# Kernel tuning notes

Hardware: AMD Instinct MI355X
Metric: run time of the kernel (lower is better)

The kernel has to match this reference:

```python
import jax, jax.numpy as jnp
import numpy as np
import math

N_NODES = 100000
N_EDGES = 3200000
NFEAT = 512
NHID = 256
NCLASS = 16
NLAYERS = 8
LAMDA = 0.5
ALPHA = 0.1


def setup_inputs() -> dict:
    key = jax.random.key(0)
    ks = jax.random.split(key, 10)
    x = jax.random.normal(ks[0], (N_NODES, NFEAT), dtype=jnp.float32)
    edge_src = jax.random.randint(ks[1], (N_EDGES,), 0, N_NODES, dtype=jnp.int32)
    edge_dst = jax.random.randint(ks[2], (N_EDGES,), 0, N_NODES, dtype=jnp.int32)
    edge_w = jax.random.uniform(ks[3], (N_EDGES,), dtype=jnp.float32)
    # fcs[0]: Linear(nfeat, nhidden); fcs[1]: Linear(nhidden, nclass)
    s0 = 1.0 / math.sqrt(NFEAT)
    w0 = jax.random.uniform(ks[4], (NFEAT, NHID), minval=-s0, maxval=s0, dtype=jnp.float32)
    b0 = jax.random.uniform(ks[5], (NHID,), minval=-s0, maxval=s0, dtype=jnp.float32)
    # conv weights: uniform(-1/sqrt(out_features), +), out_features = nhidden
    sc = 1.0 / math.sqrt(NHID)
    conv_w = jax.random.uniform(ks[6], (NLAYERS, NHID, NHID), minval=-sc, maxval=sc, dtype=jnp.float32)
    w1 = jax.random.uniform(ks[7], (NHID, NCLASS), minval=-sc, maxval=sc, dtype=jnp.float32)
    b1 = jax.random.uniform(ks[8], (NCLASS,), minval=-sc, maxval=sc, dtype=jnp.float32)
    return {"x": x, "edge_src": edge_src, "edge_dst": edge_dst, "edge_w": edge_w,
            "w0": w0, "b0": b0, "conv_w": conv_w, "w1": w1, "b1": b1}


def _spmm(edge_src, edge_dst, edge_w, h):
    # torch.spmm(adj, h): out[i] = sum_j adj[i,j] * h[j], adj in COO (dst=row, src=col)
    msgs = edge_w[:, None] * h[edge_src]            # [E, H] irregular gather
    return jax.ops.segment_sum(msgs, edge_dst, num_segments=h.shape[0])


def reference(x, edge_src, edge_dst, edge_w, w0, b0, conv_w, w1, b1):
    # eval mode: F.dropout is identity
    h = jax.nn.relu(x @ w0 + b0)                    # [N, NHID]
    h0 = h
    for i in range(NLAYERS):
        theta = math.log(LAMDA / (i + 1) + 1.0)
        hi = _spmm(edge_src, edge_dst, edge_w, h)   # sparse aggregate
        support = (1.0 - ALPHA) * hi + ALPHA * h0   # initial residual (GCNII)
        out = theta * (support @ conv_w[i]) + (1.0 - theta) * support
        h = jax.nn.relu(out + h)                    # layer residual
    return jax.nn.sigmoid(h @ w1 + b1)              # [N, NCLASS]
```

## Files before the change

### kernel.cpp

```cpp
#include <hip/hip_runtime.h>
#include <math.h>

#define N_NODES 100000
#define N_EDGES 3200000
#define NFEAT 512
#define NHID 256
#define NCLASS 16
#define NLAYERS 8

#define SCAN_CHUNK 1024
#define NB ((N_NODES + SCAN_CHUNK - 1) / SCAN_CHUNK)

__global__ void k_hist(const int* __restrict__ dst, int* __restrict__ cnt) {
  int i = blockIdx.x * 256 + threadIdx.x;
  if (i < N_EDGES) atomicAdd(&cnt[dst[i]], 1);
}

__global__ void k_blocksum(const int* __restrict__ cnt, int* __restrict__ bs) {
  __shared__ int red[256];
  int b = blockIdx.x, t = threadIdx.x;
  int s = 0;
  int base = b * SCAN_CHUNK;
  for (int j = 0; j < 4; ++j) {
    int i = base + t + j * 256;
    if (i < N_NODES) s += cnt[i];
  }
  red[t] = s;
  __syncthreads();
  for (int off = 128; off > 0; off >>= 1) {
    if (t < off) red[t] += red[t + off];
    __syncthreads();
  }
  if (t == 0) bs[b] = red[0];
}

__global__ void k_scan_top(int* __restrict__ bs, int* __restrict__ rp) {
  if (threadIdx.x == 0) {
    int run = 0;
    for (int b = 0; b < NB; ++b) { int v = bs[b]; bs[b] = run; run += v; }
    rp[N_NODES] = run;
  }
}

__global__ void k_scan_write(const int* __restrict__ cnt, const int* __restrict__ bs,
                             int* __restrict__ rp) {
  __shared__ int tot[256];
  int b = blockIdx.x, t = threadIdx.x;
  int base = b * SCAN_CHUNK + t * 4;
  int v0 = 0, v1 = 0, v2 = 0, v3 = 0;
  if (base + 0 < N_NODES) v0 = cnt[base + 0];
  if (base + 1 < N_NODES) v1 = cnt[base + 1];
  if (base + 2 < N_NODES) v2 = cnt[base + 2];
  if (base + 3 < N_NODES) v3 = cnt[base + 3];
  int tsum = v0 + v1 + v2 + v3;
  tot[t] = tsum;
  __syncthreads();
  for (int off = 1; off < 256; off <<= 1) {
    int v = 0;
    if (t >= off) v = tot[t - off];
    __syncthreads();
    if (t >= off) tot[t] += v;
    __syncthreads();
  }
  int excl = tot[t] - tsum + bs[b];
  if (base + 0 < N_NODES) rp[base + 0] = excl;
  if (base + 1 < N_NODES) rp[base + 1] = excl + v0;
  if (base + 2 < N_NODES) rp[base + 2] = excl + v0 + v1;
  if (base + 3 < N_NODES) rp[base + 3] = excl + v0 + v1 + v2;
}

__global__ void k_fill(const int* __restrict__ src, const int* __restrict__ dst,
                       const float* __restrict__ w, const int* __restrict__ rp,
                       int* __restrict__ fill, int* __restrict__ col,
                       float* __restrict__ val) {
  int i = blockIdx.x * 256 + threadIdx.x;
  if (i < N_EDGES) {
    int d = dst[i];
    int pos = rp[d] + atomicAdd(&fill[d], 1);
    col[pos] = src[i];
    val[pos] = w[i];
  }
}

__global__ __launch_bounds__(256)
void k_spmm_half(const int* __restrict__ rp, const int* __restrict__ col,
                 const float* __restrict__ val, const float* __restrict__ h,
                 const float* __restrict__ h0, float* __restrict__ sup, int f0) {
  int wave = threadIdx.x >> 6;
  int lane = threadIdx.x & 63;
  int node = blockIdx.x * 4 + wave;
  if (node >= N_NODES) return;
  int e0 = rp[node], e1 = rp[node + 1];
  const float2* __restrict__ hv = (const float2*)h;
  int fo = (f0 >> 1) + lane;

  float2 a0 = make_float2(0.f, 0.f);
  float2 a1 = make_float2(0.f, 0.f);
  float2 a2 = make_float2(0.f, 0.f);
  float2 a3 = make_float2(0.f, 0.f);

  int e = e0;
  for (; e + 4 <= e1; e += 4) {
    int s0 = col[e], s1 = col[e + 1], s2 = col[e + 2], s3 = col[e + 3];
    float w0 = val[e], w1 = val[e + 1], w2 = val[e + 2], w3 = val[e + 3];
    float2 v0 = hv[(size_t)s0 * 128 + fo];
    float2 v1 = hv[(size_t)s1 * 128 + fo];
    float2 v2 = hv[(size_t)s2 * 128 + fo];
    float2 v3 = hv[(size_t)s3 * 128 + fo];
    a0.x += w0 * v0.x; a0.y += w0 * v0.y;
    a1.x += w1 * v1.x; a1.y += w1 * v1.y;
    a2.x += w2 * v2.x; a2.y += w2 * v2.y;
    a3.x += w3 * v3.x; a3.y += w3 * v3.y;
  }
  for (; e < e1; ++e) {
    int s0 = col[e];
    float w0 = val[e];
    float2 v0 = hv[(size_t)s0 * 128 + fo];
    a0.x += w0 * v0.x; a0.y += w0 * v0.y;
  }

  float2 acc;
  acc.x = (a0.x + a1.x) + (a2.x + a3.x);
  acc.y = (a0.y + a1.y) + (a2.y + a3.y);

  float2 z = ((const float2*)h0)[(size_t)node * 128 + fo];
  float2 o;
  o.x = 0.9f * acc.x + 0.1f * z.x;
  o.y = 0.9f * acc.y + 0.1f * z.y;
  ((float2*)sup)[(size_t)node * 128 + fo] = o;
}

template <int MODE>
__global__ __launch_bounds__(256)
void k_gemm(const float* __restrict__ A, const float* __restrict__ W, int K,
            const float* __restrict__ bias, const float* __restrict__ hin,
            float* __restrict__ out1, float* __restrict__ out2, float theta) {
  __shared__ float As[16][128];
  __shared__ float Bs[16][128];
  int bm = blockIdx.x * 128, bn = blockIdx.y * 128;
  int tid = threadIdx.x;
  int tx = tid & 15, ty = tid >> 4;
  float acc[8][8];
#pragma unroll
  for (int i = 0; i < 8; ++i)
#pragma unroll
    for (int j = 0; j < 8; ++j) acc[i][j] = 0.f;

  for (int kc = 0; kc < K; kc += 16) {
#pragma unroll
    for (int it = 0; it < 2; ++it) {
      int idx = tid + it * 256;
      int m = idx >> 2, q = (idx & 3) * 4;
      int gm = bm + m;
      float4 f = make_float4(0.f, 0.f, 0.f, 0.f);
      if (gm < N_NODES) f = *(const float4*)&A[(size_t)gm * K + kc + q];
      As[q + 0][m] = f.x; As[q + 1][m] = f.y; As[q + 2][m] = f.z; As[q + 3][m] = f.w;
    }
#pragma unroll
    for (int it = 0; it < 2; ++it) {
      int idx = tid + it * 256;
      int kk = idx >> 5, nq = (idx & 31) * 4;
      *(float4*)&Bs[kk][nq] = *(const float4*)&W[(size_t)(kc + kk) * NHID + bn + nq];
    }
    __syncthreads();
#pragma unroll
    for (int k = 0; k < 16; ++k) {
      float a[8], b[8];
      *(float4*)&a[0] = *(const float4*)&As[k][ty * 8];
      *(float4*)&a[4] = *(const float4*)&As[k][ty * 8 + 4];
      *(float4*)&b[0] = *(const float4*)&Bs[k][tx * 4];
      *(float4*)&b[4] = *(const float4*)&Bs[k][tx * 4 + 64];
#pragma unroll
      for (int i = 0; i < 8; ++i)
#pragma unroll
        for (int j = 0; j < 8; ++j) acc[i][j] += a[i] * b[j];
    }
    __syncthreads();
  }

  int c0 = bn + tx * 4, c1 = bn + 64 + tx * 4;
#pragma unroll
  for (int i = 0; i < 8; ++i) {
    int gm = bm + ty * 8 + i;
    if (gm >= N_NODES) continue;
    size_t r0 = (size_t)gm * NHID + c0;
    size_t r1 = (size_t)gm * NHID + c1;
    if (MODE == 0) {
      float4 bb0 = *(const float4*)&bias[c0];
      float4 bb1 = *(const float4*)&bias[c1];
      float4 o0, o1;
      o0.x = fmaxf(acc[i][0] + bb0.x, 0.f);
      o0.y = fmaxf(acc[i][1] + bb0.y, 0.f);
      o0.z = fmaxf(acc[i][2] + bb0.z, 0.f);
      o0.w = fmaxf(acc[i][3] + bb0.w, 0.f);
      o1.x = fmaxf(acc[i][4] + bb1.x, 0.f);
      o1.y = fmaxf(acc[i][5] + bb1.y, 0.f);
      o1.z = fmaxf(acc[i][6] + bb1.z, 0.f);
      o1.w = fmaxf(acc[i][7] + bb1.w, 0.f);
      *(float4*)&out1[r0] = o0;
      *(float4*)&out1[r1] = o1;
      *(float4*)&out2[r0] = o0;
      *(float4*)&out2[r1] = o1;
    } else {
      float omt = 1.f - theta;
      float4 s0 = *(const float4*)&A[r0];
      float4 s1 = *(const float4*)&A[r1];
      float4 h0v = *(const float4*)&hin[r0];
      float4 h1v = *(const float4*)&hin[r1];
      float4 o0, o1;
      o0.x = fmaxf(theta * acc[i][0] + omt * s0.x + h0v.x, 0.f);
      o0.y = fmaxf(theta * acc[i][1] + omt * s0.y + h0v.y, 0.f);
      o0.z = fmaxf(theta * acc[i][2] + omt * s0.z + h0v.z, 0.f);
      o0.w = fmaxf(theta * acc[i][3] + omt * s0.w + h0v.w, 0.f);
      o1.x = fmaxf(theta * acc[i][4] + omt * s1.x + h1v.x, 0.f);
      o1.y = fmaxf(theta * acc[i][5] + omt * s1.y + h1v.y, 0.f);
      o1.z = fmaxf(theta * acc[i][6] + omt * s1.z + h1v.z, 0.f);
      o1.w = fmaxf(theta * acc[i][7] + omt * s1.w + h1v.w, 0.f);
      *(float4*)&out1[r0] = o0;
      *(float4*)&out1[r1] = o1;
    }
  }
}

__global__ __launch_bounds__(256)
void k_final(const float* __restrict__ h, const float* __restrict__ w1,
             const float* __restrict__ b1, float* __restrict__ out) {
  __shared__ float ws[NHID * NCLASS];
  int t = threadIdx.x;
  for (int i = t; i < NHID * NCLASS; i += 256) ws[i] = w1[i];
  __syncthreads();
  int node = blockIdx.x * 16 + (t >> 4);
  int c = t & 15;
  if (node >= N_NODES) return;
  float acc = b1[c];
  const float* hr = &h[(size_t)node * NHID];
  for (int k = 0; k < NHID; k += 4) {
    float4 hv = *(const float4*)&hr[k];
    acc += hv.x * ws[(k + 0) * NCLASS + c];
    acc += hv.y * ws[(k + 1) * NCLASS + c];
    acc += hv.z * ws[(k + 2) * NCLASS + c];
    acc += hv.w * ws[(k + 3) * NCLASS + c];
  }
  out[(size_t)node * NCLASS + c] = 1.f / (1.f + __expf(-acc));
}

extern "C" void kernel_launch(void* const* d_in, const int* in_sizes, int n_in,
                              void* d_out, int out_size, void* d_ws, size_t ws_size,
                              hipStream_t stream) {
  const float* x        = (const float*)d_in[0];
  const int*   edge_src = (const int*)d_in[1];
  const int*   edge_dst = (const int*)d_in[2];
  const float* edge_w   = (const float*)d_in[3];
  const float* w0       = (const float*)d_in[4];
  const float* b0       = (const float*)d_in[5];
  const float* conv_w   = (const float*)d_in[6];
  const float* w1       = (const float*)d_in[7];
  const float* b1       = (const float*)d_in[8];
  float* out = (float*)d_out;

  char* ws = (char*)d_ws;
  size_t off = 0;
  auto alloc = [&](size_t bytes) {
    size_t o = off;
    off = (off + bytes + 255) & ~(size_t)255;
    return (void*)(ws + o);
  };
  float* h   = (float*)alloc((size_t)N_NODES * NHID * 4);
  float* h0  = (float*)alloc((size_t)N_NODES * NHID * 4);
  float* sup = (float*)alloc((size_t)N_NODES * NHID * 4);
  int*   rp  = (int*)alloc((size_t)(N_NODES + 1) * 4);
  int*   cnt = (int*)alloc((size_t)N_NODES * 4);
  int*   col = (int*)alloc((size_t)N_EDGES * 4);
  float* val = (float*)alloc((size_t)N_EDGES * 4);
  int*   bs  = (int*)alloc((size_t)NB * 4);
  (void)ws_size;

  hipMemsetAsync(cnt, 0, (size_t)N_NODES * 4, stream);
  k_hist<<<(N_EDGES + 255) / 256, 256, 0, stream>>>(edge_dst, cnt);
  k_blocksum<<<NB, 256, 0, stream>>>(cnt, bs);
  k_scan_top<<<1, 64, 0, stream>>>(bs, rp);
  k_scan_write<<<NB, 256, 0, stream>>>(cnt, bs, rp);
  hipMemsetAsync(cnt, 0, (size_t)N_NODES * 4, stream);
  k_fill<<<(N_EDGES + 255) / 256, 256, 0, stream>>>(edge_src, edge_dst, edge_w, rp,
                                                    cnt, col, val);

  dim3 g0((N_NODES + 127) / 128, NHID / 128);
  k_gemm<0><<<g0, 256, 0, stream>>>(x, w0, NFEAT, b0, nullptr, h, h0, 0.f);

  for (int i = 0; i < NLAYERS; ++i) {
    float theta = logf(0.5f / (float)(i + 1) + 1.0f);
    k_spmm_half<<<(N_NODES + 3) / 4, 256, 0, stream>>>(rp, col, val, h, h0, sup, 0);
    k_spmm_half<<<(N_NODES + 3) / 4, 256, 0, stream>>>(rp, col, val, h, h0, sup, 128);
    const float* cw = conv_w + (size_t)i * NHID * NHID;
    k_gemm<1><<<g0, 256, 0, stream>>>(sup, cw, NHID, nullptr, h, h, nullptr, theta);
  }

  k_final<<<(N_NODES + 15) / 16, 256, 0, stream>>>(h, w1, b1, out);
}
```

Before: 5.943 ms.

## Double-buffer GEMM tiles with async LDS loads and widen block to full hidden width

The GEMM kernel now covers all 256 output columns per block, so each 128-row tile of A is loaded once instead of twice. It double-buffers A and W tiles in shared memory, prefetching the next K-slice while the current one is computed. W is copied straight into LDS with global_load_lds. Each thread now holds a 128-float accumulator, which raises register pressure against the requested two blocks per CU, and shared memory use triples.

```diff
diff --git a/kernel.cpp b/kernel.cpp
--- a/kernel.cpp
+++ b/kernel.cpp
@@ -130,94 +130,129 @@
   ((float2*)sup)[(size_t)node * 128 + fo] = o;
 }
 
+__device__ __forceinline__ void async_copy16(void* lds_dst, const void* gsrc) {
+  __builtin_amdgcn_global_load_lds(
+      (const __attribute__((address_space(1))) unsigned int*)gsrc,
+      (__attribute__((address_space(3))) unsigned int*)lds_dst, 16, 0, 0);
+}
+
 template <int MODE>
-__global__ __launch_bounds__(256)
+__global__ __launch_bounds__(256, 2)
 void k_gemm(const float* __restrict__ A, const float* __restrict__ W, int K,
             const float* __restrict__ bias, const float* __restrict__ hin,
             float* __restrict__ out1, float* __restrict__ out2, float theta) {
-  __shared__ float As[16][128];
-  __shared__ float Bs[16][128];
-  int bm = blockIdx.x * 128, bn = blockIdx.y * 128;
-  int tid = threadIdx.x;
-  int tx = tid & 15, ty = tid >> 4;
-  float acc[8][8];
+  __shared__ float As[2][16][128];
+  __shared__ float Bs[2][16][256];
+  const int bm = blockIdx.x * 128;
+  const int tid = threadIdx.x;
+  const int tx = tid & 15, ty = tid >> 4;
+  const int wave = tid >> 6, lane = tid & 63;
+
+  float acc[8][16];
 #pragma unroll
   for (int i = 0; i < 8; ++i)
 #pragma unroll
-    for (int j = 0; j < 8; ++j) acc[i][j] = 0.f;
-
-  for (int kc = 0; kc < K; kc += 16) {
-#pragma unroll
-    for (int it = 0; it < 2; ++it) {
-      int idx = tid + it * 256;
-      int m = idx >> 2, q = (idx & 3) * 4;
-      int gm = bm + m;
-      float4 f = make_float4(0.f, 0.f, 0.f, 0.f);
-      if (gm < N_NODES) f = *(const float4*)&A[(size_t)gm * K + kc + q];
-      As[q + 0][m] = f.x; As[q + 1][m] = f.y; As[q + 2][m] = f.z; As[q + 3][m] = f.w;
-    }
-#pragma unroll
-    for (int it = 0; it < 2; ++it) {
-      int idx = tid + it * 256;
-      int kk = idx >> 5, nq = (idx & 31) * 4;
-      *(float4*)&Bs[kk][nq] = *(const float4*)&W[(size_t)(kc + kk) * NHID + bn + nq];
-    }
-    __syncthreads();
+    for (int j = 0; j < 16; ++j) acc[i][j] = 0.f;
+
+  const int sm = tid >> 1;
+  const int sq = (tid & 1) * 8;
+  const int gms = bm + sm;
+  const bool mok = gms < N_NODES;
+  const float* arow = A + (size_t)gms * K;
+
+  const int nt = K / 16;
+
+  {
+#pragma unroll
+    for (int j = 0; j < 4; ++j) {
+      const int ch = j * 4 + wave;
+      async_copy16((char*)&Bs[0][0][0] + ch * 1024,
+                   (const char*)W + (size_t)ch * 1024 + lane * 16);
+    }
+    float4 f0 = make_float4(0.f, 0.f, 0.f, 0.f), f1 = f0;
+    if (mok) {
+      f0 = *(const float4*)&arow[sq];
+      f1 = *(const float4*)&arow[sq + 4];
+    }
+    As[0][sq + 0][sm] = f0.x; As[0][sq + 1][sm] = f0.y;
+    As[0][sq + 2][sm] = f0.z; As[0][sq + 3][sm] = f0.w;
+    As[0][sq + 4][sm] = f1.x; As[0][sq + 5][sm] = f1.y;
+    As[0][sq + 6][sm] = f1.z; As[0][sq + 7][sm] = f1.w;
+    __syncthreads();
+  }
+
+  int c = 0;
+  for (int t = 0; t < nt; ++t) {
+    float4 f0, f1;
+    const bool pf = (t + 1 < nt);
+    if (pf) {
+      const size_t boff = (size_t)(t + 1) * 16384;
+#pragma unroll
+      for (int j = 0; j < 4; ++j) {
+        const int ch = j * 4 + wave;
+        async_copy16((char*)&Bs[c ^ 1][0][0] + ch * 1024,
+                     (const char*)W + boff + (size_t)ch * 1024 + lane * 16);
+      }
+      f0 = make_float4(0.f, 0.f, 0.f, 0.f); f1 = f0;
+      const int kn = (t + 1) * 16;
+      if (mok) {
+        f0 = *(const float4*)&arow[kn + sq];
+        f1 = *(const float4*)&arow[kn + sq + 4];
+      }
+    }
 #pragma unroll
     for (int k = 0; k < 16; ++k) {
-      float a[8], b[8];
-      *(float4*)&a[0] = *(const float4*)&As[k][ty * 8];
-      *(float4*)&a[4] = *(const float4*)&As[k][ty * 8 + 4];
-      *(float4*)&b[0] = *(const float4*)&Bs[k][tx * 4];
-      *(float4*)&b[4] = *(const float4*)&Bs[k][tx * 4 + 64];
+      float a[8], b[16];
+      *(float4*)&a[0] = *(const float4*)&As[c][k][ty * 8];
+      *(float4*)&a[4] = *(const float4*)&As[c][k][ty * 8 + 4];
+      *(float4*)&b[0]  = *(const float4*)&Bs[c][k][tx * 4];
+      *(float4*)&b[4]  = *(const float4*)&Bs[c][k][tx * 4 + 64];
+      *(float4*)&b[8]  = *(const float4*)&Bs[c][k][tx * 4 + 128];
+      *(float4*)&b[12] = *(const float4*)&Bs[c][k][tx * 4 + 192];
 #pragma unroll
       for (int i = 0; i < 8; ++i)
 #pragma unroll
-        for (int j = 0; j < 8; ++j) acc[i][j] += a[i] * b[j];
-    }
-    __syncthreads();
-  }
-
-  int c0 = bn + tx * 4, c1 = bn + 64 + tx * 4;
+        for (int j = 0; j < 16; ++j) acc[i][j] += a[i] * b[j];
+    }
+    if (pf) {
+      As[c ^ 1][sq + 0][sm] = f0.x; As[c ^ 1][sq + 1][sm] = f0.y;
+      As[c ^ 1][sq + 2][sm] = f0.z; As[c ^ 1][sq + 3][sm] = f0.w;
+      As[c ^ 1][sq + 4][sm] = f1.x; As[c ^ 1][sq + 5][sm] = f1.y;
+      As[c ^ 1][sq + 6][sm] = f1.z; As[c ^ 1][sq + 7][sm] = f1.w;
+    }
+    __syncthreads();
+    c ^= 1;
+  }
+
+  const int c0 = tx * 4;
+  const float omt = 1.f - theta;
 #pragma unroll
   for (int i = 0; i < 8; ++i) {
     int gm = bm + ty * 8 + i;
     if (gm >= N_NODES) continue;
-    size_t r0 = (size_t)gm * NHID + c0;
-    size_t r1 = (size_t)gm * NHID + c1;
-    if (MODE == 0) {
-      float4 bb0 = *(const float4*)&bias[c0];
-      float4 bb1 = *(const float4*)&bias[c1];
-      float4 o0, o1;
-      o0.x = fmaxf(acc[i][0] + bb0.x, 0.f);
-      o0.y = fmaxf(acc[i][1] + bb0.y, 0.f);
-      o0.z = fmaxf(acc[i][2] + bb0.z, 0.f);
-      o0.w = fmaxf(acc[i][3] + bb0.w, 0.f);
-      o1.x = fmaxf(acc[i][4] + bb1.x, 0.f);
-      o1.y = fmaxf(acc[i][5] + bb1.y, 0.f);
-      o1.z = fmaxf(acc[i][6] + bb1.z, 0.f);
-      o1.w = fmaxf(acc[i][7] + bb1.w, 0.f);
-      *(float4*)&out1[r0] = o0;
-      *(float4*)&out1[r1] = o1;
-      *(float4*)&out2[r0] = o0;
-      *(float4*)&out2[r1] = o1;
-    } else {
-      float omt = 1.f - theta;
-      float4 s0 = *(const float4*)&A[r0];
-      float4 s1 = *(const float4*)&A[r1];
-      float4 h0v = *(const float4*)&hin[r0];
-      float4 h1v = *(const float4*)&hin[r1];
-      float4 o0, o1;
-      o0.x = fmaxf(theta * acc[i][0] + omt * s0.x + h0v.x, 0.f);
-      o0.y = fmaxf(theta * acc[i][1] + omt * s0.y + h0v.y, 0.f);
-      o0.z = fmaxf(theta * acc[i][2] + omt * s0.z + h0v.z, 0.f);
-      o0.w = fmaxf(theta * acc[i][3] + omt * s0.w + h0v.w, 0.f);
-      o1.x = fmaxf(theta * acc[i][4] + omt * s1.x + h1v.x, 0.f);
-      o1.y = fmaxf(theta * acc[i][5] + omt * s1.y + h1v.y, 0.f);
-      o1.z = fmaxf(theta * acc[i][6] + omt * s1.z + h1v.z, 0.f);
-      o1.w = fmaxf(theta * acc[i][7] + omt * s1.w + h1v.w, 0.f);
-      *(float4*)&out1[r0] = o0;
-      *(float4*)&out1[r1] = o1;
+    size_t base = (size_t)gm * NHID;
+#pragma unroll
+    for (int q = 0; q < 4; ++q) {
+      size_t r = base + c0 + q * 64;
+      if (MODE == 0) {
+        float4 bb = *(const float4*)&bias[c0 + q * 64];
+        float4 o;
+        o.x = fmaxf(acc[i][q * 4 + 0] + bb.x, 0.f);
+        o.y = fmaxf(acc[i][q * 4 + 1] + bb.y, 0.f);
+        o.z = fmaxf(acc[i][q * 4 + 2] + bb.z, 0.f);
+        o.w = fmaxf(acc[i][q * 4 + 3] + bb.w, 0.f);
+        *(float4*)&out1[r] = o;
+        *(float4*)&out2[r] = o;
+      } else {
+        float4 s = *(const float4*)&A[r];
+        float4 hv = *(const float4*)&hin[r];
+        float4 o;
+        o.x = fmaxf(theta * acc[i][q * 4 + 0] + omt * s.x + hv.x, 0.f);
+        o.y = fmaxf(theta * acc[i][q * 4 + 1] + omt * s.y + hv.y, 0.f);
+        o.z = fmaxf(theta * acc[i][q * 4 + 2] + omt * s.z + hv.z, 0.f);
+        o.w = fmaxf(theta * acc[i][q * 4 + 3] + omt * s.w + hv.w, 0.f);
+        *(float4*)&out1[r] = o;
+      }
     }
   }
 }
@@ -284,15 +319,15 @@
   k_fill<<<(N_EDGES + 255) / 256, 256, 0, stream>>>(edge_src, edge_dst, edge_w, rp,
                                                     cnt, col, val);
 
-  dim3 g0((N_NODES + 127) / 128, NHID / 128);
-  k_gemm<0><<<g0, 256, 0, stream>>>(x, w0, NFEAT, b0, nullptr, h, h0, 0.f);
+  int gblocks = (N_NODES + 127) / 128;
+  k_gemm<0><<<gblocks, 256, 0, stream>>>(x, w0, NFEAT, b0, nullptr, h, h0, 0.f);
 
   for (int i = 0; i < NLAYERS; ++i) {
     float theta = logf(0.5f / (float)(i + 1) + 1.0f);
     k_spmm_half<<<(N_NODES + 3) / 4, 256, 0, stream>>>(rp, col, val, h, h0, sup, 0);
     k_spmm_half<<<(N_NODES + 3) / 4, 256, 0, stream>>>(rp, col, val, h, h0, sup, 128);
     const float* cw = conv_w + (size_t)i * NHID * NHID;
-    k_gemm<1><<<g0, 256, 0, stream>>>(sup, cw, NHID, nullptr, h, h, nullptr, theta);
+    k_gemm<1><<<gblocks, 256, 0, stream>>>(sup, cw, NHID, nullptr, h, h, nullptr, theta);
   }
 
   k_final<<<(N_NODES + 15) / 16, 256, 0, stream>>>(h, w1, b1, out);
```

New measurement: 22.32 ms. 276% more time.

## Replace FP32 SIMT GEMMs with split-bf16 MFMA GEMMs

Applied to the files above, without the earlier changes.

Swaps the scalar FP32 register-tiled GEMM for a matrix-core kernel that uses bf16 MFMA 16x16x32 instructions. Each operand is split into bf16 hi and lo parts and combined through three products (hh, hl, lh) to keep close to FP32 accuracy. Weights are split and transposed once per call by a new kernel, while activations are split on the fly while staging into LDS. The aim is to move the dense GEMM work from vector ALUs to matrix cores. In exchange it adds conversion ALU work, triples the MFMA count, and uses a scalar, less-coalesced epilogue.

```diff
diff --git a/kernel.cpp b/kernel.cpp
--- a/kernel.cpp
+++ b/kernel.cpp
@@ -10,6 +10,18 @@
 
 #define SCAN_CHUNK 1024
 #define NB ((N_NODES + SCAN_CHUNK - 1) / SCAN_CHUNK)
+
+typedef float f32x4 __attribute__((ext_vector_type(4)));
+typedef short s16x8 __attribute__((ext_vector_type(8)));
+
+__device__ __forceinline__ unsigned short bf16_rne(float f) {
+  unsigned u = __float_as_uint(f);
+  unsigned r = 0x7fffu + ((u >> 16) & 1u);
+  return (unsigned short)((u + r) >> 16);
+}
+__device__ __forceinline__ float bf16_tof(unsigned short h) {
+  return __uint_as_float(((unsigned)h) << 16);
+}
 
 __global__ void k_hist(const int* __restrict__ dst, int* __restrict__ cnt) {
   int i = blockIdx.x * 256 + threadIdx.x;
@@ -130,94 +142,127 @@
   ((float2*)sup)[(size_t)node * 128 + fo] = o;
 }
 
+__global__ void k_splitw(const float* __restrict__ W, unsigned short* __restrict__ hi,
+                         unsigned short* __restrict__ lo, int K) {
+  int mat = blockIdx.y;
+  const float* Wm = W + (size_t)mat * K * NHID;
+  unsigned short* hm = hi + (size_t)mat * K * NHID;
+  unsigned short* lm = lo + (size_t)mat * K * NHID;
+  int idx = blockIdx.x * 256 + threadIdx.x;
+  if (idx >= K * NHID) return;
+  int k = idx >> 8;
+  int n = idx & 255;
+  float f = Wm[idx];
+  unsigned short h = bf16_rne(f);
+  unsigned short l = bf16_rne(f - bf16_tof(h));
+  hm[(size_t)n * K + k] = h;
+  lm[(size_t)n * K + k] = l;
+}
+
+#define PADK 40
+
 template <int MODE>
 __global__ __launch_bounds__(256)
-void k_gemm(const float* __restrict__ A, const float* __restrict__ W, int K,
-            const float* __restrict__ bias, const float* __restrict__ hin,
-            float* __restrict__ out1, float* __restrict__ out2, float theta) {
-  __shared__ float As[16][128];
-  __shared__ float Bs[16][128];
-  int bm = blockIdx.x * 128, bn = blockIdx.y * 128;
-  int tid = threadIdx.x;
-  int tx = tid & 15, ty = tid >> 4;
-  float acc[8][8];
-#pragma unroll
-  for (int i = 0; i < 8; ++i)
-#pragma unroll
-    for (int j = 0; j < 8; ++j) acc[i][j] = 0.f;
-
-  for (int kc = 0; kc < K; kc += 16) {
-#pragma unroll
-    for (int it = 0; it < 2; ++it) {
-      int idx = tid + it * 256;
-      int m = idx >> 2, q = (idx & 3) * 4;
-      int gm = bm + m;
+void k_gemm_mfma(const float* __restrict__ A, const unsigned short* __restrict__ Bh_g,
+                 const unsigned short* __restrict__ Bl_g, int K,
+                 const float* __restrict__ bias, const float* __restrict__ hin,
+                 float* __restrict__ out1, float* __restrict__ out2, float theta) {
+  __shared__ unsigned short Ah[128][PADK];
+  __shared__ unsigned short Al[128][PADK];
+  __shared__ unsigned short Bh[128][PADK];
+  __shared__ unsigned short Bl[128][PADK];
+  const int bm = blockIdx.x * 128, bn = blockIdx.y * 128;
+  const int tid = threadIdx.x;
+  const int lane = tid & 63, wave = tid >> 6;
+  const int wr = (wave >> 1) * 64;
+  const int wc = (wave & 1) * 64;
+  const int l16 = lane & 15, lk = lane >> 4;
+
+  f32x4 acc[4][4];
+#pragma unroll
+  for (int i = 0; i < 4; ++i)
+#pragma unroll
+    for (int j = 0; j < 4; ++j)
+#pragma unroll
+      for (int q = 0; q < 4; ++q) acc[i][j][q] = 0.f;
+
+  const int srow = tid >> 3;
+  const int skq = (tid & 7) * 4;
+
+  for (int kc = 0; kc < K; kc += 32) {
+#pragma unroll
+    for (int it = 0; it < 4; ++it) {
+      int row = srow + it * 32;
+      int gm = bm + row;
       float4 f = make_float4(0.f, 0.f, 0.f, 0.f);
-      if (gm < N_NODES) f = *(const float4*)&A[(size_t)gm * K + kc + q];
-      As[q + 0][m] = f.x; As[q + 1][m] = f.y; As[q + 2][m] = f.z; As[q + 3][m] = f.w;
+      if (gm < N_NODES) f = *(const float4*)&A[(size_t)gm * K + kc + skq];
+      unsigned short h0 = bf16_rne(f.x), h1 = bf16_rne(f.y);
+      unsigned short h2 = bf16_rne(f.z), h3 = bf16_rne(f.w);
+      ushort4 hv = make_ushort4(h0, h1, h2, h3);
+      ushort4 lv = make_ushort4(bf16_rne(f.x - bf16_tof(h0)),
+                                bf16_rne(f.y - bf16_tof(h1)),
+                                bf16_rne(f.z - bf16_tof(h2)),
+                                bf16_rne(f.w - bf16_tof(h3)));
+      *(ushort4*)&Ah[row][skq] = hv;
+      *(ushort4*)&Al[row][skq] = lv;
     }
 #pragma unroll
-    for (int it = 0; it < 2; ++it) {
-      int idx = tid + it * 256;
-      int kk = idx >> 5, nq = (idx & 31) * 4;
-      *(float4*)&Bs[kk][nq] = *(const float4*)&W[(size_t)(kc + kk) * NHID + bn + nq];
+    for (int it = 0; it < 4; ++it) {
+      int row = srow + it * 32;
+      size_t go = (size_t)(bn + row) * K + kc + skq;
+      *(ushort4*)&Bh[row][skq] = *(const ushort4*)&Bh_g[go];
+      *(ushort4*)&Bl[row][skq] = *(const ushort4*)&Bl_g[go];
     }
     __syncthreads();
-#pragma unroll
-    for (int k = 0; k < 16; ++k) {
-      float a[8], b[8];
-      *(float4*)&a[0] = *(const float4*)&As[k][ty * 8];
-      *(float4*)&a[4] = *(const float4*)&As[k][ty * 8 + 4];
-      *(float4*)&b[0] = *(const float4*)&Bs[k][tx * 4];
-      *(float4*)&b[4] = *(const float4*)&Bs[k][tx * 4 + 64];
-#pragma unroll
-      for (int i = 0; i < 8; ++i)
-#pragma unroll
-        for (int j = 0; j < 8; ++j) acc[i][j] += a[i] * b[j];
+
+    s16x8 ah[4], al[4], bh[4], bl[4];
+#pragma unroll
+    for (int i = 0; i < 4; ++i) {
+      ah[i] = *(const s16x8*)&Ah[wr + i * 16 + l16][lk * 8];
+      al[i] = *(const s16x8*)&Al[wr + i * 16 + l16][lk * 8];
+      bh[i] = *(const s16x8*)&Bh[wc + i * 16 + l16][lk * 8];
+      bl[i] = *(const s16x8*)&Bl[wc + i * 16 + l16][lk * 8];
     }
-    __syncthreads();
-  }
-
-  int c0 = bn + tx * 4, c1 = bn + 64 + tx * 4;
-#pragma unroll
-  for (int i = 0; i < 8; ++i) {
-    int gm = bm + ty * 8 + i;
-    if (gm >= N_NODES) continue;
-    size_t r0 = (size_t)gm * NHID + c0;
-    size_t r1 = (size_t)gm * NHID + c1;
-    if (MODE == 0) {
-      float4 bb0 = *(const float4*)&bias[c0];
-      float4 bb1 = *(const float4*)&bias[c1];
-      float4 o0, o1;
-      o0.x = fmaxf(acc[i][0] + bb0.x, 0.f);
-      o0.y = fmaxf(acc[i][1] + bb0.y, 0.f);
-      o0.z = fmaxf(acc[i][2] + bb0.z, 0.f);
-      o0.w = fmaxf(acc[i][3] + bb0.w, 0.f);
-      o1.x = fmaxf(acc[i][4] + bb1.x, 0.f);
-      o1.y = fmaxf(acc[i][5] + bb1.y, 0.f);
-      o1.z = fmaxf(acc[i][6] + bb1.z, 0.f);
-      o1.w = fmaxf(acc[i][7] + bb1.w, 0.f);
-      *(float4*)&out1[r0] = o0;
-      *(float4*)&out1[r1] = o1;
-      *(float4*)&out2[r0] = o0;
-      *(float4*)&out2[r1] = o1;
-    } else {
-      float omt = 1.f - theta;
-      float4 s0 = *(const float4*)&A[r0];
-      float4 s1 = *(const float4*)&A[r1];
-      float4 h0v = *(const float4*)&hin[r0];
-      float4 h1v = *(const float4*)&hin[r1];
-      float4 o0, o1;
-      o0.x = fmaxf(theta * acc[i][0] + omt * s0.x + h0v.x, 0.f);
-      o0.y = fmaxf(theta * acc[i][1] + omt * s0.y + h0v.y, 0.f);
-      o0.z = fmaxf(theta * acc[i][2] + omt * s0.z + h0v.z, 0.f);
-      o0.w = fmaxf(theta * acc[i][3] + omt * s0.w + h0v.w, 0.f);
-      o1.x = fmaxf(theta * acc[i][4] + omt * s1.x + h1v.x, 0.f);
-      o1.y = fmaxf(theta * acc[i][5] + omt * s1.y + h1v.y, 0.f);
-      o1.z = fmaxf(theta * acc[i][6] + omt * s1.z + h1v.z, 0.f);
-      o1.w = fmaxf(theta * acc[i][7] + omt * s1.w + h1v.w, 0.f);
-      *(float4*)&out1[r0] = o0;
-      *(float4*)&out1[r1] = o1;
+#pragma unroll
+    for (int i = 0; i < 4; ++i)
+#pragma unroll
+      for (int j = 0; j < 4; ++j)
+        acc[i][j] = __builtin_amdgcn_mfma_f32_16x16x32_bf16(ah[i], bh[j], acc[i][j], 0, 0, 0);
+#pragma unroll
+    for (int i = 0; i < 4; ++i)
+#pragma unroll
+      for (int j = 0; j < 4; ++j)
+        acc[i][j] = __builtin_amdgcn_mfma_f32_16x16x32_bf16(ah[i], bl[j], acc[i][j], 0, 0, 0);
+#pragma unroll
+    for (int i = 0; i < 4; ++i)
+#pragma unroll
+      for (int j = 0; j < 4; ++j)
+        acc[i][j] = __builtin_amdgcn_mfma_f32_16x16x32_bf16(al[i], bh[j], acc[i][j], 0, 0, 0);
+    __syncthreads();
+  }
+
+  const float omt = 1.f - theta;
+#pragma unroll
+  for (int i = 0; i < 4; ++i) {
+#pragma unroll
+    for (int j = 0; j < 4; ++j) {
+      int gn = bn + wc + j * 16 + l16;
+#pragma unroll
+      for (int q = 0; q < 4; ++q) {
+        int gm = bm + wr + i * 16 + lk * 4 + q;
+        if (gm >= N_NODES) continue;
+        size_t r = (size_t)gm * NHID + gn;
+        float v = acc[i][j][q];
+        if (MODE == 0) {
+          float o = fmaxf(v + bias[gn], 0.f);
+          out1[r] = o;
+          out2[r] = o;
+        } else {
+          float s = A[r];
+          float o = fmaxf(theta * v + omt * s + hin[r], 0.f);
+          out1[r] = o;
+        }
+      }
     }
   }
 }
@@ -273,26 +318,34 @@
   int*   col = (int*)alloc((size_t)N_EDGES * 4);
   float* val = (float*)alloc((size_t)N_EDGES * 4);
   int*   bs  = (int*)alloc((size_t)NB * 4);
+  unsigned short* w0t_hi = (unsigned short*)alloc((size_t)NFEAT * NHID * 2);
+  unsigned short* w0t_lo = (unsigned short*)alloc((size_t)NFEAT * NHID * 2);
+  unsigned short* cwt_hi = (unsigned short*)alloc((size_t)NLAYERS * NHID * NHID * 2);
+  unsigned short* cwt_lo = (unsigned short*)alloc((size_t)NLAYERS * NHID * NHID * 2);
   (void)ws_size;
 
-  hipMemsetAsync(cnt, 0, (size_t)N_NODES * 4, stream);
+  (void)hipMemsetAsync(cnt, 0, (size_t)N_NODES * 4, stream);
   k_hist<<<(N_EDGES + 255) / 256, 256, 0, stream>>>(edge_dst, cnt);
   k_blocksum<<<NB, 256, 0, stream>>>(cnt, bs);
   k_scan_top<<<1, 64, 0, stream>>>(bs, rp);
   k_scan_write<<<NB, 256, 0, stream>>>(cnt, bs, rp);
-  hipMemsetAsync(cnt, 0, (size_t)N_NODES * 4, stream);
+  (void)hipMemsetAsync(cnt, 0, (size_t)N_NODES * 4, stream);
   k_fill<<<(N_EDGES + 255) / 256, 256, 0, stream>>>(edge_src, edge_dst, edge_w, rp,
                                                     cnt, col, val);
 
+  k_splitw<<<dim3((NFEAT * NHID + 255) / 256, 1), 256, 0, stream>>>(w0, w0t_hi, w0t_lo, NFEAT);
+  k_splitw<<<dim3((NHID * NHID + 255) / 256, NLAYERS), 256, 0, stream>>>(conv_w, cwt_hi, cwt_lo, NHID);
+
   dim3 g0((N_NODES + 127) / 128, NHID / 128);
-  k_gemm<0><<<g0, 256, 0, stream>>>(x, w0, NFEAT, b0, nullptr, h, h0, 0.f);
+  k_gemm_mfma<0><<<g0, 256, 0, stream>>>(x, w0t_hi, w0t_lo, NFEAT, b0, nullptr, h, h0, 0.f);
 
   for (int i = 0; i < NLAYERS; ++i) {
     float theta = logf(0.5f / (float)(i + 1) + 1.0f);
     k_spmm_half<<<(N_NODES + 3) / 4, 256, 0, stream>>>(rp, col, val, h, h0, sup, 0);
     k_spmm_half<<<(N_NODES + 3) / 4, 256, 0, stream>>>(rp, col, val, h, h0, sup, 128);
-    const float* cw = conv_w + (size_t)i * NHID * NHID;
-    k_gemm<1><<<g0, 256, 0, stream>>>(sup, cw, NHID, nullptr, h, h, nullptr, theta);
+    const unsigned short* whi = cwt_hi + (size_t)i * NHID * NHID;
+    const unsigned short* wlo = cwt_lo + (size_t)i * NHID * NHID;
+    k_gemm_mfma<1><<<g0, 256, 0, stream>>>(sup, whi, wlo, NHID, nullptr, h, h, nullptr, theta);
   }
 
   k_final<<<(N_NODES + 15) / 16, 256, 0, stream>>>(h, w1, b1, out);
```

Measured after the change: 5.855 ms. Within noise of the previous version (-1.5%).
